# Performance work log

Measured on AMD Instinct MI355X. Metric: run time of the kernel, lower is better.

The kernel has to match this reference:

```python
import jax, jax.numpy as jnp
import numpy as np

B, N, ND_, FEAT, WV = 32, 1024, 8, 2048, 300
E, T, STEPS = 20000, 2, 5
NDIM = N * ND_  # 8192


def setup_inputs() -> dict:
    key = jax.random.key(0)
    ks = jax.random.split(key, 20)
    s = 0.02
    inputs = jax.random.normal(ks[0], (B, FEAT), jnp.float32)
    wordvecs = jax.random.normal(ks[1], (N, WV), jnp.float32)
    # unique edges per type (disjoint across types) so the scatter has no duplicate indices
    rng = np.random.default_rng(0)
    codes = rng.permutation(N * N)[: T * E].reshape(T, E)
    edge_u = (codes // N).astype(np.int32)
    edge_v = (codes % N).astype(np.int32)
    ki = np.repeat(np.arange(ND_), ND_)
    kj = np.tile(np.arange(ND_), ND_)
    mat_u = (edge_u.reshape(-1)[:, None] * ND_ + ki[None, :]).reshape(-1).astype(np.int32)
    mat_v = (edge_v.reshape(-1)[:, None] * ND_ + kj[None, :]).reshape(-1).astype(np.int32)
    p = {
        'inputs': inputs, 'wordvecs': wordvecs,
        'edge_u': jnp.asarray(edge_u), 'edge_v': jnp.asarray(edge_v),
        'mat_u': jnp.asarray(mat_u), 'mat_v': jnp.asarray(mat_v),
        # Inputnet: Linear(feat+wv -> 512), Linear(512 -> node_dim)
        'W_in1': jax.random.normal(ks[2], (512, FEAT + WV), jnp.float32) * s,
        'b_in1': jnp.zeros((512,), jnp.float32),
        'W_in2': jax.random.normal(ks[3], (ND_, 512), jnp.float32) * s,
        'b_in2': jnp.zeros((ND_,), jnp.float32),
        # embnet: Linear(wv -> 50)
        'W_emb': jax.random.normal(ks[4], (50, WV), jnp.float32) * s,
        'b_emb': jnp.zeros((50,), jnp.float32),
        # relnets: one (50, 50*nd^2) matrix per edge type
        'rel_mats': jax.random.normal(ks[5], (T, 50, 50 * ND_ * ND_), jnp.float32) * s,
        # GRUCell(node_dim, node_dim)
        'W_ih': jax.random.normal(ks[6], (3 * ND_, ND_), jnp.float32) * s,
        'W_hh': jax.random.normal(ks[7], (3 * ND_, ND_), jnp.float32) * s,
        'b_ih': jnp.zeros((3 * ND_,), jnp.float32),
        'b_hh': jnp.zeros((3 * ND_,), jnp.float32),
        # outnet: Linear(nd -> 20), ReLU, Linear(20 -> 1)
        'W_o1': jax.random.normal(ks[8], (20, ND_), jnp.float32) * s,
        'b_o1': jnp.zeros((20,), jnp.float32),
        'W_o2': jax.random.normal(ks[9], (1, 20), jnp.float32) * s,
        'b_o2': jnp.zeros((1,), jnp.float32),
    }
    return p


def reference(inputs, wordvecs, edge_u, edge_v, mat_u, mat_v,
              W_in1, b_in1, W_in2, b_in2, W_emb, b_emb, rel_mats,
              W_ih, W_hh, b_ih, b_hh, W_o1, b_o1, W_o2, b_o2):
    nd = W_in2.shape[0]
    n_nodes = wordvecs.shape[0]
    ndim = n_nodes * nd
    bsz = inputs.shape[0]

    # Inputnet: per-(image, node) feature -> initial hidden state [B, N*nd]
    f = jnp.concatenate([
        jnp.broadcast_to(inputs[:, None, :], (bsz, n_nodes, inputs.shape[1])),
        jnp.broadcast_to(wordvecs[None, :, :], (bsz, n_nodes, wordvecs.shape[1])),
    ], axis=-1).reshape(bsz * n_nodes, -1)
    h = jax.nn.relu(f @ W_in1.T + b_in1) @ W_in2.T + b_in2  # [B*N, nd]
    hidden = h.reshape(bsz, ndim)

    # edge weights via Relnet per edge type
    embs = wordvecs @ W_emb.T + b_emb  # [N, 50]
    ws = []
    for t in range(rel_mats.shape[0]):
        ue = embs[edge_u[t]]  # [E, 50]
        ve = embs[edge_v[t]]  # [E, 50]
        tmp = (ue @ rel_mats[t]).reshape(ue.shape[0], embs.shape[1], nd * nd)
        ws.append(jnp.einsum('ed,edk->ek', ve, tmp))  # [E, nd^2]
    weights = jnp.concatenate(ws, axis=0).reshape(-1)

    # scatter into dense propagation matrix
    P = jnp.zeros((ndim, ndim), jnp.float32).at[mat_u, mat_v].set(weights)
    norm = jnp.sqrt(jnp.sum(P * P, axis=1))  # row L2 norms [ndim]
    norm = norm + (norm == 0).astype(P.dtype)
    P = P / norm  # NOTE: torch broadcasting divides COLUMNS by row norms (faithful)

    def gru(x, hc):
        gi = x @ W_ih.T + b_ih
        gh = hc @ W_hh.T + b_hh
        ir, iz, inn = jnp.split(gi, 3, axis=-1)
        hr, hz, hn = jnp.split(gh, 3, axis=-1)
        r = jax.nn.sigmoid(ir + hr)
        z = jax.nn.sigmoid(iz + hz)
        n = jnp.tanh(inn + r * hn)
        return (1.0 - z) * n + z * hc

    hiddens = [hidden]
    for _ in range(STEPS):
        x = jnp.tanh(hidden @ P.T)  # [B, ndim]
        hidden = gru(x.reshape(-1, nd), hidden.reshape(-1, nd)).reshape(bsz, ndim)
        hiddens.append(hidden)
    states = jnp.stack(hiddens, axis=1)  # [B, STEPS+1, ndim]

    o = jax.nn.relu(states.reshape(-1, nd) @ W_o1.T + b_o1) @ W_o2.T + b_o2  # [B*(S+1)*N, 1]
    logits = o.reshape(bsz, STEPS + 1, n_nodes).transpose(0, 2, 1)  # [B, N, S+1]
    return logits
```

## Files before the change

kernel.cpp:

```cpp
#include <hip/hip_runtime.h>
#include <math.h>

constexpr int B = 32, N = 1024, ND = 8, FEAT = 2048, WVD = 300;
constexpr int E = 20000, T = 2, STEPS = 5;
constexpr int NDIM = N * ND;
constexpr int H1 = 512;
constexpr int W1C = FEAT + WVD;
constexpr int EMB = 50;
constexpr int RC = EMB * ND * ND;
constexpr int KH = 150;
constexpr int CAP = 64;
constexpr int SEG = 16;
constexpr int SEGLEN = E / SEG;

constexpr int G_KA   = 512;
constexpr int G_W1T  = 16 * 10;
constexpr int G_EMB  = N * 25 / 4;
constexpr int G_SEGH = T * N * SEG / 4;
constexpr int F1_TOT = G_KA + G_W1T + G_EMB + G_SEGH;

constexpr int G_ARED = 8;
constexpr int G_WV   = 512;
constexpr int G_AHAT = 13 * 32 * T;
constexpr int F2_TOT = G_ARED + G_WV + G_AHAT;

constexpr int G_SCAT = T * N * SEG / 4;
constexpr int F3_TOT = G_SCAT + N;

__global__ __launch_bounds__(256) void k_f1(
        const int* eu, int* segcnt,
        const float* inp, const float* W1, float* partA, float* W1T,
        const float* wv, const float* We, const float* be,
        float* embs, float* embsT) {
    __shared__ float smem[8 * 260];
    int tid = threadIdx.x;
    int blk = blockIdx.x;
    if (blk < G_KA) {
        int c = tid & 7, b = tid >> 3;
        int c0 = (blk & 63) * 8;
        int ks = blk >> 6;
        int kt = ks * 256;
        {
            int r = tid >> 5, cb = (tid & 31) * 8;
            const float* src = W1 + (size_t)(c0 + r) * W1C + kt + cb;
            float4 a0 = *(const float4*)src;
            float4 a1 = *(const float4*)(src + 4);
            *(float4*)&smem[r * 260 + cb] = a0;
            *(float4*)&smem[r * 260 + cb + 4] = a1;
        }
        __syncthreads();
        const float* xr = inp + (size_t)b * FEAT + kt;
        float acc = 0.f;
#pragma unroll 8
        for (int k4 = 0; k4 < 64; k4++) {
            float4 x = *(const float4*)(xr + k4 * 4);
            float4 w = *(const float4*)&smem[c * 260 + k4 * 4];
            acc += x.x * w.x + x.y * w.y + x.z * w.z + x.w * w.w;
        }
        partA[(size_t)ks * (H1 * B) + (c0 + c) * B + b] = acc;
    } else if (blk < G_KA + G_W1T) {
        int lb = blk - G_KA;
        int c0 = (lb % 16) * 32, k0 = (lb / 16) * 32;
        float (*tile)[33] = (float(*)[33])smem;
        int kl = tid & 31, cl4 = tid >> 5;
#pragma unroll
        for (int p = 0; p < 4; p++) {
            int c = cl4 + p * 8;
            int k = k0 + kl;
            if (k < WVD) tile[c][kl] = W1[(size_t)(c0 + c) * W1C + FEAT + k];
        }
        __syncthreads();
        int cl = tid & 31, kl4 = tid >> 5;
#pragma unroll
        for (int p = 0; p < 4; p++) {
            int kk = kl4 + p * 8;
            int k = k0 + kk;
            if (k < WVD) W1T[(size_t)k * H1 + c0 + cl] = tile[cl][kk];
        }
    } else if (blk < G_KA + G_W1T + G_EMB) {
        int lb = blk - G_KA - G_W1T;
        int wid = lb * 4 + (tid >> 6);
        int lane = tid & 63;
        int n = wid / 25, cp = wid - n * 25;
        int c0 = cp * 2;
        const float* xr = wv + (size_t)n * WVD;
        const float* wr0 = We + (size_t)c0 * WVD;
        const float* wr1 = wr0 + WVD;
        float a0 = 0.f, a1 = 0.f;
#pragma unroll
        for (int i = 0; i < 5; i++) {
            int k = i * 64 + lane;
            if (k < WVD) {
                float x = xr[k];
                a0 += x * wr0[k];
                a1 += x * wr1[k];
            }
        }
        for (int m = 32; m; m >>= 1) {
            a0 += __shfl_xor(a0, m, 64);
            a1 += __shfl_xor(a1, m, 64);
        }
        if (lane == 0) {
            float v0 = a0 + be[c0], v1 = a1 + be[c0 + 1];
            embs[n * EMB + c0] = v0;
            embs[n * EMB + c0 + 1] = v1;
            embsT[c0 * N + n] = v0;
            embsT[(c0 + 1) * N + n] = v1;
        }
    } else {
        int lb = blk - G_KA - G_W1T - G_EMB;
        int wid = lb * 4 + (tid >> 6);
        int lane = tid & 63;
        int t = wid >> 14, u = (wid >> 4) & (N - 1), seg = wid & (SEG - 1);
        const int* eut = eu + t * E;
        int e0 = seg * SEGLEN, e1 = e0 + SEGLEN, cnt = 0;
        for (int c = e0; c < e1; c += 64) {
            int e = c + lane;
            bool ok = (e < e1) && (eut[e] == u);
            cnt += __popcll(__ballot(ok));
        }
        if (lane == 0) segcnt[wid] = cnt;
    }
}

__global__ __launch_bounds__(256) void k_f2(
        const float* partA, float* AbT,
        const float* wv, const float* W1T, float* Wp,
        const float* embsT, const float* RMbase, float* Ahat) {
    __shared__ float smemf[1800];
    int tid = threadIdx.x, blk = blockIdx.x;
    if (blk < G_ARED) {
        int cb = blk * 2048 + tid * 8;
        float4 s0 = {0, 0, 0, 0}, s1 = {0, 0, 0, 0};
#pragma unroll
        for (int ks = 0; ks < 8; ks++) {
            const float* p = partA + (size_t)ks * (H1 * B) + cb;
            float4 a = *(const float4*)p;
            float4 b4 = *(const float4*)(p + 4);
            s0.x += a.x; s0.y += a.y; s0.z += a.z; s0.w += a.w;
            s1.x += b4.x; s1.y += b4.y; s1.z += b4.z; s1.w += b4.w;
        }
        *(float4*)(AbT + cb) = s0;
        *(float4*)(AbT + cb + 4) = s1;
    } else if (blk < G_ARED + G_WV) {
        int lb = blk - G_ARED;
        int kh = lb >> 8;
        int rem = lb & 255;
        int c = (rem & 1) * 256 + tid;
        int n0 = (rem >> 1) * 8;
        int kb = kh * KH;
        float (*el)[8] = (float(*)[8])smemf;
        for (int idx = tid; idx < 8 * KH; idx += 256) {
            int j = idx / KH, k = idx - j * KH;
            el[k][j] = wv[(size_t)(n0 + j) * WVD + kb + k];
        }
        __syncthreads();
        float acc[8] = {};
#pragma unroll 5
        for (int k = 0; k < KH; k++) {
            float r = W1T[(size_t)(kb + k) * H1 + c];
            float4 e0 = *(const float4*)&el[k][0];
            float4 e1 = *(const float4*)&el[k][4];
            acc[0] += e0.x * r; acc[1] += e0.y * r;
            acc[2] += e0.z * r; acc[3] += e0.w * r;
            acc[4] += e1.x * r; acc[5] += e1.y * r;
            acc[6] += e1.z * r; acc[7] += e1.w * r;
        }
        float* wout = Wp + (size_t)kh * N * H1;
#pragma unroll
        for (int j = 0; j < 8; j++) wout[(size_t)(n0 + j) * H1 + c] = acc[j];
    } else {
        int lb = blk - G_ARED - G_WV;
        int t = lb / 416, r = lb % 416;
        int bx = r % 13, by = r / 13;
        const float* RM = RMbase + (size_t)t * EMB * RC;
        float* Ah = Ahat + (size_t)t * N * RC;
        int n0 = by * 32;
        float (*el)[36] = (float(*)[36])smemf;
        for (int idx = tid; idx < EMB * 32; idx += 256)
            el[idx >> 5][idx & 31] = embsT[(idx >> 5) * N + n0 + (idx & 31)];
        __syncthreads();
        int mi = bx * 256 + (tid & 63) * 4;
        int ni = (tid >> 6) * 8;
        if (mi < RC) {
            float acc[8][4] = {};
#pragma unroll 2
            for (int c = 0; c < EMB; c++) {
                float4 rm = *(const float4*)(RM + (size_t)c * RC + mi);
                float4 e0 = *(const float4*)&el[c][ni];
                float4 e1 = *(const float4*)&el[c][ni + 4];
                float ev[8] = {e0.x, e0.y, e0.z, e0.w, e1.x, e1.y, e1.z, e1.w};
#pragma unroll
                for (int j = 0; j < 8; j++) {
                    acc[j][0] += ev[j] * rm.x;
                    acc[j][1] += ev[j] * rm.y;
                    acc[j][2] += ev[j] * rm.z;
                    acc[j][3] += ev[j] * rm.w;
                }
            }
#pragma unroll
            for (int j = 0; j < 8; j++) {
                float4 o = {acc[j][0], acc[j][1], acc[j][2], acc[j][3]};
                *(float4*)(Ah + (size_t)(n0 + ni + j) * RC + mi) = o;
            }
        }
    }
}

__global__ __launch_bounds__(256) void k_f3(
        const int* eu, const int* ev, const int* segcnt, int* sv,
        const float* AbT, const float* Wp, const float* b1,
        const float* W2, const float* b2, float* sT0) {
    __shared__ float smem[6656];
    int tid = threadIdx.x, blk = blockIdx.x;
    if (blk < G_SCAT) {
        int wid = blk * 4 + (tid >> 6);
        int lane = tid & 63;
        int t = wid >> 14, u = (wid >> 4) & (N - 1), seg = wid & (SEG - 1);
        const int* eut = eu + t * E;
        const int* evt = ev + t * E;
        int row = t * N + u;
        int pre = 0;
        for (int j = 0; j < seg; j++) pre += segcnt[row * SEG + j];
        int base = row * CAP + pre;
        int e0 = seg * SEGLEN, e1 = e0 + SEGLEN, cnt = 0;
        for (int c = e0; c < e1; c += 64) {
            int e = c + lane;
            bool ok = (e < e1) && (eut[e] == u);
            unsigned long long m = __ballot(ok);
            if (ok) {
                int rank = __popcll(m & ((1ull << lane) - 1));
                sv[base + cnt + rank] = evt[e];
            }
            cnt += __popcll(m);
        }
    } else {
        int n = blk - G_SCAT;
        float* w2s  = smem;
        float* wvs  = smem + 4096;
        float* part = smem + 4608;
        for (int idx = tid; idx < 8 * H1; idx += 256) w2s[idx] = W2[idx];
        for (int idx = tid; idx < H1; idx += 256)
            wvs[idx] = Wp[(size_t)n * H1 + idx]
                     + Wp[(size_t)N * H1 + (size_t)n * H1 + idx] + b1[idx];
        __syncthreads();
        int b = tid & 31, s = tid >> 5;
        float acc[8] = {};
        for (int i = 0; i < 64; i++) {
            int c = s * 64 + i;
            float tv = fmaxf(AbT[c * 32 + b] + wvs[c], 0.f);
#pragma unroll
            for (int ki = 0; ki < 8; ki++) acc[ki] += tv * w2s[ki * H1 + c];
        }
#pragma unroll
        for (int ki = 0; ki < 8; ki++) part[s * 256 + ki * 32 + b] = acc[ki];
        __syncthreads();
        int ki2 = tid >> 5, b2i = tid & 31;
        float tot = b2[ki2];
#pragma unroll
        for (int s2 = 0; s2 < 8; s2++) tot += part[s2 * 256 + ki2 * 32 + b2i];
        sT0[(size_t)n * 256 + tid] = tot;
    }
}

__global__ __launch_bounds__(256) void k_f4(
        const int* segcnt, const int* sv, int* counts,
        const float* embs, const float* Ahat, float* wbuf, float* inorm) {
    __shared__ float AL[RC];
    __shared__ int vl[T][CAP];
    __shared__ int cl[T];
    int tid = threadIdx.x;
    int u = blockIdx.x;
    int w = tid >> 6, k = tid & 63;
    if (tid < T) {
        int row = tid * N + u;
        int c = 0;
#pragma unroll
        for (int j = 0; j < SEG; j++) c += segcnt[row * SEG + j];
        cl[tid] = c;
        counts[row] = c;
    }
    __syncthreads();
    int cnts[T];
#pragma unroll
    for (int t = 0; t < T; t++) {
        cnts[t] = cl[t];
        if (tid < CAP && tid < cnts[t])
            vl[t][tid] = sv[(size_t)(t * N + u) * CAP + tid];
    }
    float ssq = 0.f;
    for (int t = 0; t < T; t++) {
        __syncthreads();
        for (int idx = tid; idx < RC; idx += 256)
            AL[idx] = Ahat[((size_t)t * N + u) * RC + idx];
        __syncthreads();
        int cnt = cnts[t];
        size_t base = (size_t)(t * N + u) * CAP;
        for (int i = w; i < cnt; i += 4) {
            int v = vl[t][i];
            const float* vr = embs + v * EMB;
            float acc = 0.f;
#pragma unroll 10
            for (int d = 0; d < EMB; d++) acc += vr[d] * AL[d * 64 + k];
            wbuf[(base + i) * 64 + k] = acc;
            ssq += acc * acc;
        }
    }
    __syncthreads();
    AL[w * 64 + k] = ssq;
    __syncthreads();
    if (tid < 64) {
        float tot = AL[tid] + AL[64 + tid] + AL[128 + tid] + AL[192 + tid];
        tot += __shfl_xor(tot, 1, 64);
        tot += __shfl_xor(tot, 2, 64);
        tot += __shfl_xor(tot, 4, 64);
        int ki = tid >> 3, kj = tid & 7;
        if (kj == 0) {
            float nv = sqrtf(tot);
            if (nv == 0.f) nv = 1.f;
            inorm[u * ND + ki] = 1.0f / nv;
        }
    }
}

__global__ __launch_bounds__(256) void k_step(
        const int* counts, const int* sv,
        const float* wbuf, const float* inorm, const float* sT, int s,
        const float* W_ih, const float* W_hh, const float* b_ih, const float* b_hh,
        const float* Wo1, const float* bo1, const float* Wo2, const float* bo2,
        float* sOut, float* out, int last) {
    __shared__ float xs[256], hs[256], hfin[256];
    __shared__ float wih[192], whh[192];
    __shared__ float w1s[160], b1s[20], w2s[20];
    __shared__ float res[8][33];
    int tid = threadIdx.x;
    int u = blockIdx.x;
    int ki = tid >> 5, b = tid & 31;
    if (tid < 192) { wih[tid] = W_ih[tid]; whh[tid] = W_hh[tid]; }
    if (last) {
        if (tid < 160) w1s[tid] = Wo1[tid];
        if (tid < 20) { b1s[tid] = bo1[tid]; w2s[tid] = Wo2[tid]; }
    }
    const float* sIn = sT + (size_t)s * NDIM * B;
    float hown = sIn[((size_t)u * 8 + ki) * B + b];
    float acc = 0.f;
    for (int t = 0; t < T; t++) {
        int row = t * N + u;
        int cnt = counts[row];
        size_t base = (size_t)row * CAP;
        int i = 0;
        for (; i + 1 < cnt; i += 2) {
            size_t s0 = base + i, s1 = base + i + 1;
            int v0 = sv[s0], v1 = sv[s1];
            const float* wp0 = wbuf + s0 * 64 + ki * 8;
            const float* wp1 = wbuf + s1 * 64 + ki * 8;
            float4 wa0 = *(const float4*)wp0;
            float4 wb0 = *(const float4*)(wp0 + 4);
            float4 wa1 = *(const float4*)wp1;
            float4 wb1 = *(const float4*)(wp1 + 4);
            const float* ip0 = inorm + v0 * ND;
            const float* ip1 = inorm + v1 * ND;
            const float* hp0 = sIn + (size_t)v0 * 256 + b;
            const float* hp1 = sIn + (size_t)v1 * 256 + b;
            acc += (wa0.x * ip0[0]) * hp0[0]   + (wa0.y * ip0[1]) * hp0[32]
                 + (wa0.z * ip0[2]) * hp0[64]  + (wa0.w * ip0[3]) * hp0[96]
                 + (wb0.x * ip0[4]) * hp0[128] + (wb0.y * ip0[5]) * hp0[160]
                 + (wb0.z * ip0[6]) * hp0[192] + (wb0.w * ip0[7]) * hp0[224];
            acc += (wa1.x * ip1[0]) * hp1[0]   + (wa1.y * ip1[1]) * hp1[32]
                 + (wa1.z * ip1[2]) * hp1[64]  + (wa1.w * ip1[3]) * hp1[96]
                 + (wb1.x * ip1[4]) * hp1[128] + (wb1.y * ip1[5]) * hp1[160]
                 + (wb1.z * ip1[6]) * hp1[192] + (wb1.w * ip1[7]) * hp1[224];
        }
        if (i < cnt) {
            size_t s0 = base + i;
            int v0 = sv[s0];
            const float* wp0 = wbuf + s0 * 64 + ki * 8;
            float4 wa0 = *(const float4*)wp0;
            float4 wb0 = *(const float4*)(wp0 + 4);
            const float* ip0 = inorm + v0 * ND;
            const float* hp0 = sIn + (size_t)v0 * 256 + b;
            acc += (wa0.x * ip0[0]) * hp0[0]   + (wa0.y * ip0[1]) * hp0[32]
                 + (wa0.z * ip0[2]) * hp0[64]  + (wa0.w * ip0[3]) * hp0[96]
                 + (wb0.x * ip0[4]) * hp0[128] + (wb0.y * ip0[5]) * hp0[160]
                 + (wb0.z * ip0[6]) * hp0[192] + (wb0.w * ip0[7]) * hp0[224];
        }
    }
    float xv = tanhf(acc);
    xs[ki * 32 + b] = xv;
    hs[ki * 32 + b] = hown;
    __syncthreads();
    float gr = b_ih[ki], gz = b_ih[8 + ki], gn = b_ih[16 + ki];
    float hr = b_hh[ki], hz = b_hh[8 + ki], hn = b_hh[16 + ki];
#pragma unroll
    for (int j = 0; j < 8; j++) {
        float xj = xs[j * 32 + b], hj = hs[j * 32 + b];
        gr += wih[ki * 8 + j] * xj;
        gz += wih[(8 + ki) * 8 + j] * xj;
        gn += wih[(16 + ki) * 8 + j] * xj;
        hr += whh[ki * 8 + j] * hj;
        hz += whh[(8 + ki) * 8 + j] * hj;
        hn += whh[(16 + ki) * 8 + j] * hj;
    }
    float r = 1.f / (1.f + expf(-(gr + hr)));
    float z = 1.f / (1.f + expf(-(gz + hz)));
    float nn = tanhf(gn + r * hn);
    float hnew = (1.f - z) * nn + z * hown;
    if (!last) {
        sOut[((size_t)u * 8 + ki) * B + b] = hnew;
        return;
    }
    hfin[ki * 32 + b] = hnew;
    __syncthreads();
    int s6 = tid >> 5, bb = tid & 31;
    if (s6 < 6) {
        float x[8];
#pragma unroll
        for (int kk = 0; kk < 8; kk++)
            x[kk] = (s6 < STEPS)
                ? sT[((size_t)s6 * NDIM + u * 8 + kk) * B + bb]
                : hfin[kk * 32 + bb];
        float accv = bo2[0];
#pragma unroll
        for (int j = 0; j < 20; j++) {
            float h = b1s[j];
#pragma unroll
            for (int kk = 0; kk < 8; kk++) h += w1s[j * 8 + kk] * x[kk];
            h = fmaxf(h, 0.f);
            accv += w2s[j] * h;
        }
        res[s6][bb] = accv;
    }
    __syncthreads();
    if (tid < 192) {
        int b_w = tid / 6, s_w = tid - b_w * 6;
        out[(size_t)b_w * ((STEPS + 1) * N) + u * (STEPS + 1) + s_w] = res[s_w][b_w];
    }
}

extern "C" void kernel_launch(void* const* d_in, const int* in_sizes, int n_in,
                              void* d_out, int out_size, void* d_ws, size_t ws_size,
                              hipStream_t stream) {
    const float* inputs   = (const float*)d_in[0];
    const float* wordvecs = (const float*)d_in[1];
    const int*   edge_u   = (const int*)d_in[2];
    const int*   edge_v   = (const int*)d_in[3];
    const float* W_in1 = (const float*)d_in[6];
    const float* b_in1 = (const float*)d_in[7];
    const float* W_in2 = (const float*)d_in[8];
    const float* b_in2 = (const float*)d_in[9];
    const float* W_emb = (const float*)d_in[10];
    const float* b_emb = (const float*)d_in[11];
    const float* rel_mats = (const float*)d_in[12];
    const float* W_ih = (const float*)d_in[13];
    const float* W_hh = (const float*)d_in[14];
    const float* b_ih = (const float*)d_in[15];
    const float* b_hh = (const float*)d_in[16];
    const float* W_o1 = (const float*)d_in[17];
    const float* b_o1 = (const float*)d_in[18];
    const float* W_o2 = (const float*)d_in[19];
    const float* b_o2 = (const float*)d_in[20];
    float* out = (float*)d_out;

    char* ws = (char*)d_ws;
    size_t off = 0;
    auto alloc = [&](size_t bytes) -> void* {
        void* p = ws + off;
        off = (off + bytes + 255) & ~(size_t)255;
        return p;
    };
    int* segcnt    = (int*)alloc((size_t)T * N * SEG * 4);
    int* counts    = (int*)alloc(2048 * 4);
    int* sv        = (int*)alloc((size_t)T * N * CAP * 4);
    float* inorm   = (float*)alloc((size_t)NDIM * 4);
    float* partA   = (float*)alloc((size_t)8 * H1 * B * 4);
    float* AbT     = (float*)alloc((size_t)H1 * B * 4);
    float* W1T     = (float*)alloc((size_t)WVD * H1 * 4);
    float* Wp      = (float*)alloc((size_t)2 * N * H1 * 4);
    float* embs    = (float*)alloc((size_t)N * EMB * 4);
    float* embsT   = (float*)alloc((size_t)EMB * N * 4);
    float* Ahat    = (float*)alloc((size_t)T * N * RC * 4);
    float* wbuf    = (float*)alloc((size_t)T * N * CAP * 64 * 4);
    float* sT      = (float*)alloc((size_t)(STEPS + 1) * NDIM * B * 4);

    k_f1<<<F1_TOT, 256, 0, stream>>>(edge_u, segcnt, inputs, W_in1, partA, W1T,
                                     wordvecs, W_emb, b_emb, embs, embsT);
    k_f2<<<F2_TOT, 256, 0, stream>>>(partA, AbT, wordvecs, W1T, Wp,
                                     embsT, rel_mats, Ahat);
    k_f3<<<F3_TOT, 256, 0, stream>>>(edge_u, edge_v, segcnt, sv,
                                     AbT, Wp, b_in1, W_in2, b_in2, sT);
    k_f4<<<N, 256, 0, stream>>>(segcnt, sv, counts, embs, Ahat, wbuf, inorm);

    for (int s = 0; s < STEPS; s++) {
        int last = (s == STEPS - 1) ? 1 : 0;
        k_step<<<N, 256, 0, stream>>>(counts, sv, wbuf, inorm, sT, s,
                                      W_ih, W_hh, b_ih, b_hh,
                                      W_o1, b_o1, W_o2, b_o2,
                                      sT + (size_t)(s + 1) * NDIM * B, out, last);
    }
}
```

Before: 265.5 us.

## Fuse edge-weight and GRU step kernels into one cooperative persistent kernel

Replaces the k_f4 launch and the five per-step k_step launches with a single cooperative kernel of 512 blocks, each handling two nodes, separated by grid-wide syncs. This removes the launch gaps between the six kernels and keeps the final hidden state in shared memory for the output MLP. k_f3's input-net tail also processes four nodes per block instead of one. In exchange, each block does twice the sequential work, grid.sync has its own cost, and the old path is kept as a fallback if the cooperative launch fails.

```diff
diff --git a/kernel.cpp b/kernel.cpp
--- a/kernel.cpp
+++ b/kernel.cpp
@@ -1,5 +1,8 @@
 #include <hip/hip_runtime.h>
+#include <hip/hip_cooperative_groups.h>
 #include <math.h>
+
+namespace cg = cooperative_groups;
 
 constexpr int B = 32, N = 1024, ND = 8, FEAT = 2048, WVD = 300;
 constexpr int E = 20000, T = 2, STEPS = 5;
@@ -12,6 +15,7 @@
 constexpr int CAP = 64;
 constexpr int SEG = 16;
 constexpr int SEGLEN = E / SEG;
+constexpr int NBLK = 512;
 
 constexpr int G_KA   = 512;
 constexpr int G_W1T  = 16 * 10;
@@ -25,7 +29,8 @@
 constexpr int F2_TOT = G_ARED + G_WV + G_AHAT;
 
 constexpr int G_SCAT = T * N * SEG / 4;
-constexpr int F3_TOT = G_SCAT + N;
+constexpr int G_INP  = N / 4;
+constexpr int F3_TOT = G_SCAT + G_INP;
 
 __global__ __launch_bounds__(256) void k_f1(
         const int* eu, int* segcnt,
@@ -235,31 +240,227 @@
             cnt += __popcll(m);
         }
     } else {
-        int n = blk - G_SCAT;
+        int n0 = (blk - G_SCAT) * 4;
         float* w2s  = smem;
         float* wvs  = smem + 4096;
         float* part = smem + 4608;
         for (int idx = tid; idx < 8 * H1; idx += 256) w2s[idx] = W2[idx];
-        for (int idx = tid; idx < H1; idx += 256)
-            wvs[idx] = Wp[(size_t)n * H1 + idx]
-                     + Wp[(size_t)N * H1 + (size_t)n * H1 + idx] + b1[idx];
-        __syncthreads();
         int b = tid & 31, s = tid >> 5;
-        float acc[8] = {};
-        for (int i = 0; i < 64; i++) {
-            int c = s * 64 + i;
-            float tv = fmaxf(AbT[c * 32 + b] + wvs[c], 0.f);
-#pragma unroll
-            for (int ki = 0; ki < 8; ki++) acc[ki] += tv * w2s[ki * H1 + c];
-        }
-#pragma unroll
-        for (int ki = 0; ki < 8; ki++) part[s * 256 + ki * 32 + b] = acc[ki];
-        __syncthreads();
         int ki2 = tid >> 5, b2i = tid & 31;
-        float tot = b2[ki2];
-#pragma unroll
-        for (int s2 = 0; s2 < 8; s2++) tot += part[s2 * 256 + ki2 * 32 + b2i];
-        sT0[(size_t)n * 256 + tid] = tot;
+        for (int nn = 0; nn < 4; nn++) {
+            int n = n0 + nn;
+            __syncthreads();
+            for (int idx = tid; idx < H1; idx += 256)
+                wvs[idx] = Wp[(size_t)n * H1 + idx]
+                         + Wp[(size_t)N * H1 + (size_t)n * H1 + idx] + b1[idx];
+            __syncthreads();
+            float acc[8] = {};
+            for (int i = 0; i < 64; i++) {
+                int c = s * 64 + i;
+                float tv = fmaxf(AbT[c * 32 + b] + wvs[c], 0.f);
+#pragma unroll
+                for (int ki = 0; ki < 8; ki++) acc[ki] += tv * w2s[ki * H1 + c];
+            }
+#pragma unroll
+            for (int ki = 0; ki < 8; ki++) part[s * 256 + ki * 32 + b] = acc[ki];
+            __syncthreads();
+            float tot = b2[ki2];
+#pragma unroll
+            for (int s2 = 0; s2 < 8; s2++) tot += part[s2 * 256 + ki2 * 32 + b2i];
+            sT0[(size_t)n * 256 + tid] = tot;
+        }
+    }
+}
+
+__device__ __forceinline__ float spmm_row(
+        const float* sIn, const int* sv, const float* wbuf, const float* inorm,
+        int row, int cnt, int ki, int b) {
+    float acc = 0.f;
+    size_t base = (size_t)row * CAP;
+    int i = 0;
+    for (; i + 1 < cnt; i += 2) {
+        size_t s0 = base + i, s1 = base + i + 1;
+        int v0 = sv[s0], v1 = sv[s1];
+        const float* wp0 = wbuf + s0 * 64 + ki * 8;
+        const float* wp1 = wbuf + s1 * 64 + ki * 8;
+        float4 wa0 = *(const float4*)wp0;
+        float4 wb0 = *(const float4*)(wp0 + 4);
+        float4 wa1 = *(const float4*)wp1;
+        float4 wb1 = *(const float4*)(wp1 + 4);
+        const float* ip0 = inorm + v0 * ND;
+        const float* ip1 = inorm + v1 * ND;
+        const float* hp0 = sIn + (size_t)v0 * 256 + b;
+        const float* hp1 = sIn + (size_t)v1 * 256 + b;
+        acc += (wa0.x * ip0[0]) * hp0[0]   + (wa0.y * ip0[1]) * hp0[32]
+             + (wa0.z * ip0[2]) * hp0[64]  + (wa0.w * ip0[3]) * hp0[96]
+             + (wb0.x * ip0[4]) * hp0[128] + (wb0.y * ip0[5]) * hp0[160]
+             + (wb0.z * ip0[6]) * hp0[192] + (wb0.w * ip0[7]) * hp0[224];
+        acc += (wa1.x * ip1[0]) * hp1[0]   + (wa1.y * ip1[1]) * hp1[32]
+             + (wa1.z * ip1[2]) * hp1[64]  + (wa1.w * ip1[3]) * hp1[96]
+             + (wb1.x * ip1[4]) * hp1[128] + (wb1.y * ip1[5]) * hp1[160]
+             + (wb1.z * ip1[6]) * hp1[192] + (wb1.w * ip1[7]) * hp1[224];
+    }
+    if (i < cnt) {
+        size_t s0 = base + i;
+        int v0 = sv[s0];
+        const float* wp0 = wbuf + s0 * 64 + ki * 8;
+        float4 wa0 = *(const float4*)wp0;
+        float4 wb0 = *(const float4*)(wp0 + 4);
+        const float* ip0 = inorm + v0 * ND;
+        const float* hp0 = sIn + (size_t)v0 * 256 + b;
+        acc += (wa0.x * ip0[0]) * hp0[0]   + (wa0.y * ip0[1]) * hp0[32]
+             + (wa0.z * ip0[2]) * hp0[64]  + (wa0.w * ip0[3]) * hp0[96]
+             + (wb0.x * ip0[4]) * hp0[128] + (wb0.y * ip0[5]) * hp0[160]
+             + (wb0.z * ip0[6]) * hp0[192] + (wb0.w * ip0[7]) * hp0[224];
+    }
+    return acc;
+}
+
+__global__ __launch_bounds__(256, 4) void k_steps(
+        const int* segcnt, const int* sv, const float* embs, const float* Ahat,
+        float* wbuf, float* inorm, float* sT,
+        const float* W_ih, const float* W_hh, const float* b_ih, const float* b_hh,
+        const float* Wo1, const float* bo1, const float* Wo2, const float* bo2,
+        float* out) {
+    cg::grid_group grid = cg::this_grid();
+    __shared__ float S[3400];
+    __shared__ int vl[T][CAP];
+    __shared__ int cl[T];
+    int tid = threadIdx.x;
+    int w = tid >> 6, k = tid & 63;
+    int cnts[2][T];
+
+    for (int half = 0; half < 2; half++) {
+        int u = blockIdx.x + half * NBLK;
+        __syncthreads();
+        if (tid < T) {
+            int row = tid * N + u;
+            int c = 0;
+#pragma unroll
+            for (int j = 0; j < SEG; j++) c += segcnt[row * SEG + j];
+            cl[tid] = c;
+        }
+        __syncthreads();
+#pragma unroll
+        for (int t = 0; t < T; t++) {
+            cnts[half][t] = cl[t];
+            if (tid < cnts[half][t]) vl[t][tid] = sv[(size_t)(t * N + u) * CAP + tid];
+        }
+        float ssq = 0.f;
+        for (int t = 0; t < T; t++) {
+            __syncthreads();
+            for (int idx = tid; idx < RC; idx += 256)
+                S[idx] = Ahat[((size_t)t * N + u) * RC + idx];
+            __syncthreads();
+            int cnt = cnts[half][t];
+            size_t base = (size_t)(t * N + u) * CAP;
+            for (int i = w; i < cnt; i += 4) {
+                int v = vl[t][i];
+                const float* vr = embs + v * EMB;
+                float acc = 0.f;
+#pragma unroll 10
+                for (int d = 0; d < EMB; d++) acc += vr[d] * S[d * 64 + k];
+                wbuf[(base + i) * 64 + k] = acc;
+                ssq += acc * acc;
+            }
+        }
+        __syncthreads();
+        S[w * 64 + k] = ssq;
+        __syncthreads();
+        if (tid < 64) {
+            float tot = S[tid] + S[64 + tid] + S[128 + tid] + S[192 + tid];
+            tot += __shfl_xor(tot, 1, 64);
+            tot += __shfl_xor(tot, 2, 64);
+            tot += __shfl_xor(tot, 4, 64);
+            int ki = tid >> 3, kj = tid & 7;
+            if (kj == 0) {
+                float nv = sqrtf(tot);
+                if (nv == 0.f) nv = 1.f;
+                inorm[u * ND + ki] = 1.0f / nv;
+            }
+        }
+    }
+    grid.sync();
+
+    float* xs   = S;
+    float* hs   = S + 256;
+    float* hfin = S + 512;
+    float* wih  = S + 1024;
+    float* whh  = S + 1216;
+    float* w1s  = S + 1408;
+    float* b1s  = S + 1568;
+    float* w2s  = S + 1588;
+    float (*res)[33] = (float(*)[33])(S + 1608);
+    if (tid < 192) { wih[tid] = W_ih[tid]; whh[tid] = W_hh[tid]; }
+    if (tid < 160) w1s[tid] = Wo1[tid];
+    if (tid < 20) { b1s[tid] = bo1[tid]; w2s[tid] = Wo2[tid]; }
+    __syncthreads();
+    int ki = tid >> 5, b = tid & 31;
+
+    for (int s = 0; s < STEPS; s++) {
+        const float* sIn = sT + (size_t)s * NDIM * B;
+        for (int half = 0; half < 2; half++) {
+            int u = blockIdx.x + half * NBLK;
+            float hown = sIn[((size_t)u * 8 + ki) * B + b];
+            float acc = spmm_row(sIn, sv, wbuf, inorm, u, cnts[half][0], ki, b)
+                      + spmm_row(sIn, sv, wbuf, inorm, N + u, cnts[half][1], ki, b);
+            float xv = tanhf(acc);
+            __syncthreads();
+            xs[ki * 32 + b] = xv;
+            hs[ki * 32 + b] = hown;
+            __syncthreads();
+            float gr = b_ih[ki], gz = b_ih[8 + ki], gn = b_ih[16 + ki];
+            float hr = b_hh[ki], hz = b_hh[8 + ki], hn = b_hh[16 + ki];
+#pragma unroll
+            for (int j = 0; j < 8; j++) {
+                float xj = xs[j * 32 + b], hj = hs[j * 32 + b];
+                gr += wih[ki * 8 + j] * xj;
+                gz += wih[(8 + ki) * 8 + j] * xj;
+                gn += wih[(16 + ki) * 8 + j] * xj;
+                hr += whh[ki * 8 + j] * hj;
+                hz += whh[(8 + ki) * 8 + j] * hj;
+                hn += whh[(16 + ki) * 8 + j] * hj;
+            }
+            float r = 1.f / (1.f + expf(-(gr + hr)));
+            float z = 1.f / (1.f + expf(-(gz + hz)));
+            float nn = tanhf(gn + r * hn);
+            float hnew = (1.f - z) * nn + z * hown;
+            if (s < STEPS - 1)
+                sT[(size_t)(s + 1) * NDIM * B + ((size_t)u * 8 + ki) * B + b] = hnew;
+            else
+                hfin[half * 256 + ki * 32 + b] = hnew;
+        }
+        if (s < STEPS - 1) grid.sync();
+    }
+    __syncthreads();
+
+    int s6 = tid >> 5, bb = tid & 31;
+    for (int half = 0; half < 2; half++) {
+        int u = blockIdx.x + half * NBLK;
+        __syncthreads();
+        if (s6 < 6) {
+            float x[8];
+#pragma unroll
+            for (int kk = 0; kk < 8; kk++)
+                x[kk] = (s6 < STEPS)
+                    ? sT[((size_t)s6 * NDIM + u * 8 + kk) * B + bb]
+                    : hfin[half * 256 + kk * 32 + bb];
+            float accv = bo2[0];
+#pragma unroll
+            for (int j = 0; j < 20; j++) {
+                float h = b1s[j];
+#pragma unroll
+                for (int kk = 0; kk < 8; kk++) h += w1s[j * 8 + kk] * x[kk];
+                h = fmaxf(h, 0.f);
+                accv += w2s[j] * h;
+            }
+            res[s6][bb] = accv;
+        }
+        __syncthreads();
+        if (tid < 192) {
+            int b_w = tid / 6, s_w = tid - b_w * 6;
+            out[(size_t)b_w * ((STEPS + 1) * N) + u * (STEPS + 1) + s_w] = res[s_w][b_w];
+        }
     }
 }
 
@@ -285,8 +486,7 @@
 #pragma unroll
     for (int t = 0; t < T; t++) {
         cnts[t] = cl[t];
-        if (tid < CAP && tid < cnts[t])
-            vl[t][tid] = sv[(size_t)(t * N + u) * CAP + tid];
+        if (tid < cnts[t]) vl[t][tid] = sv[(size_t)(t * N + u) * CAP + tid];
     }
     float ssq = 0.f;
     for (int t = 0; t < T; t++) {
@@ -343,48 +543,8 @@
     }
     const float* sIn = sT + (size_t)s * NDIM * B;
     float hown = sIn[((size_t)u * 8 + ki) * B + b];
-    float acc = 0.f;
-    for (int t = 0; t < T; t++) {
-        int row = t * N + u;
-        int cnt = counts[row];
-        size_t base = (size_t)row * CAP;
-        int i = 0;
-        for (; i + 1 < cnt; i += 2) {
-            size_t s0 = base + i, s1 = base + i + 1;
-            int v0 = sv[s0], v1 = sv[s1];
-            const float* wp0 = wbuf + s0 * 64 + ki * 8;
-            const float* wp1 = wbuf + s1 * 64 + ki * 8;
-            float4 wa0 = *(const float4*)wp0;
-            float4 wb0 = *(const float4*)(wp0 + 4);
-            float4 wa1 = *(const float4*)wp1;
-            float4 wb1 = *(const float4*)(wp1 + 4);
-            const float* ip0 = inorm + v0 * ND;
-            const float* ip1 = inorm + v1 * ND;
-            const float* hp0 = sIn + (size_t)v0 * 256 + b;
-            const float* hp1 = sIn + (size_t)v1 * 256 + b;
-            acc += (wa0.x * ip0[0]) * hp0[0]   + (wa0.y * ip0[1]) * hp0[32]
-                 + (wa0.z * ip0[2]) * hp0[64]  + (wa0.w * ip0[3]) * hp0[96]
-                 + (wb0.x * ip0[4]) * hp0[128] + (wb0.y * ip0[5]) * hp0[160]
-                 + (wb0.z * ip0[6]) * hp0[192] + (wb0.w * ip0[7]) * hp0[224];
-            acc += (wa1.x * ip1[0]) * hp1[0]   + (wa1.y * ip1[1]) * hp1[32]
-                 + (wa1.z * ip1[2]) * hp1[64]  + (wa1.w * ip1[3]) * hp1[96]
-                 + (wb1.x * ip1[4]) * hp1[128] + (wb1.y * ip1[5]) * hp1[160]
-                 + (wb1.z * ip1[6]) * hp1[192] + (wb1.w * ip1[7]) * hp1[224];
-        }
-        if (i < cnt) {
-            size_t s0 = base + i;
-            int v0 = sv[s0];
-            const float* wp0 = wbuf + s0 * 64 + ki * 8;
-            float4 wa0 = *(const float4*)wp0;
-            float4 wb0 = *(const float4*)(wp0 + 4);
-            const float* ip0 = inorm + v0 * ND;
-            const float* hp0 = sIn + (size_t)v0 * 256 + b;
-            acc += (wa0.x * ip0[0]) * hp0[0]   + (wa0.y * ip0[1]) * hp0[32]
-                 + (wa0.z * ip0[2]) * hp0[64]  + (wa0.w * ip0[3]) * hp0[96]
-                 + (wb0.x * ip0[4]) * hp0[128] + (wb0.y * ip0[5]) * hp0[160]
-                 + (wb0.z * ip0[6]) * hp0[192] + (wb0.w * ip0[7]) * hp0[224];
-        }
-    }
+    float acc = spmm_row(sIn, sv, wbuf, inorm, u, counts[u], ki, b)
+              + spmm_row(sIn, sv, wbuf, inorm, N + u, counts[N + u], ki, b);
     float xv = tanhf(acc);
     xs[ki * 32 + b] = xv;
     hs[ki * 32 + b] = hown;
@@ -488,13 +648,24 @@
                                      embsT, rel_mats, Ahat);
     k_f3<<<F3_TOT, 256, 0, stream>>>(edge_u, edge_v, segcnt, sv,
                                      AbT, Wp, b_in1, W_in2, b_in2, sT);
-    k_f4<<<N, 256, 0, stream>>>(segcnt, sv, counts, embs, Ahat, wbuf, inorm);
-
-    for (int s = 0; s < STEPS; s++) {
-        int last = (s == STEPS - 1) ? 1 : 0;
-        k_step<<<N, 256, 0, stream>>>(counts, sv, wbuf, inorm, sT, s,
-                                      W_ih, W_hh, b_ih, b_hh,
-                                      W_o1, b_o1, W_o2, b_o2,
-                                      sT + (size_t)(s + 1) * NDIM * B, out, last);
-    }
-}
+
+    void* args[] = {
+        (void*)&segcnt, (void*)&sv, (void*)&embs, (void*)&Ahat,
+        (void*)&wbuf, (void*)&inorm, (void*)&sT,
+        (void*)&W_ih, (void*)&W_hh, (void*)&b_ih, (void*)&b_hh,
+        (void*)&W_o1, (void*)&b_o1, (void*)&W_o2, (void*)&b_o2,
+        (void*)&out
+    };
+    hipError_t cerr = hipLaunchCooperativeKernel((const void*)k_steps, dim3(NBLK),
+                                                 dim3(256), args, 0, stream);
+    if (cerr != hipSuccess) {
+        k_f4<<<N, 256, 0, stream>>>(segcnt, sv, counts, embs, Ahat, wbuf, inorm);
+        for (int s = 0; s < STEPS; s++) {
+            int last = (s == STEPS - 1) ? 1 : 0;
+            k_step<<<N, 256, 0, stream>>>(counts, sv, wbuf, inorm, sT, s,
+                                          W_ih, W_hh, b_ih, b_hh,
+                                          W_o1, b_o1, W_o2, b_o2,
+                                          sT + (size_t)(s + 1) * NDIM * B, out, last);
+        }
+    }
+}
```

Result: slower. 653.5 us (+146.2%).

## Fuse edge scatter into per-node weight kernel and skip empty segments

Applied to the files above, without the earlier changes.

Merges the edge-list compaction pass into the per-node relation-weight kernel, so each node block builds its neighbour list in shared memory, scans only the segments that hold edges, and then computes wbuf and inorm without a separate launch. The count pass now uses 50 segments instead of 16, which makes each segment shorter and lets empty ones be skipped. The input-net blocks now process four nodes each. The aim is to remove one kernel launch, the global round trip of sv, and redundant scans over empty segments. In exchange the count pass launches more work and the fused blocks do the scan and the matvec serially.

```diff
diff --git a/kernel.cpp b/kernel.cpp
--- a/kernel.cpp
+++ b/kernel.cpp
@@ -10,7 +10,7 @@
 constexpr int RC = EMB * ND * ND;
 constexpr int KH = 150;
 constexpr int CAP = 64;
-constexpr int SEG = 16;
+constexpr int SEG = 50;
 constexpr int SEGLEN = E / SEG;
 
 constexpr int G_KA   = 512;
@@ -24,8 +24,8 @@
 constexpr int G_AHAT = 13 * 32 * T;
 constexpr int F2_TOT = G_ARED + G_WV + G_AHAT;
 
-constexpr int G_SCAT = T * N * SEG / 4;
-constexpr int F3_TOT = G_SCAT + N;
+constexpr int G_INP  = N / 4;
+constexpr int F3_TOT = N + G_INP;
 
 __global__ __launch_bounds__(256) void k_f1(
         const int* eu, int* segcnt,
@@ -111,7 +111,9 @@
         int lb = blk - G_KA - G_W1T - G_EMB;
         int wid = lb * 4 + (tid >> 6);
         int lane = tid & 63;
-        int t = wid >> 14, u = (wid >> 4) & (N - 1), seg = wid & (SEG - 1);
+        int t = wid / (N * SEG);
+        int rem = wid - t * (N * SEG);
+        int u = rem / SEG, seg = rem - u * SEG;
         const int* eut = eu + t * E;
         int e0 = seg * SEGLEN, e1 = e0 + SEGLEN, cnt = 0;
         for (int c = e0; c < e1; c += 64) {
@@ -119,7 +121,7 @@
             bool ok = (e < e1) && (eut[e] == u);
             cnt += __popcll(__ballot(ok));
         }
-        if (lane == 0) segcnt[wid] = cnt;
+        if (lane == 0) segcnt[(t * N + u) * SEG + seg] = cnt;
     }
 }
 
@@ -208,117 +210,132 @@
 }
 
 __global__ __launch_bounds__(256) void k_f3(
-        const int* eu, const int* ev, const int* segcnt, int* sv,
+        const int* eu, const int* ev, const int* segcnt,
+        const float* embs, const float* Ahat, float* wbuf, float* inorm,
+        int* counts, int* sv,
         const float* AbT, const float* Wp, const float* b1,
         const float* W2, const float* b2, float* sT0) {
     __shared__ float smem[6656];
-    int tid = threadIdx.x, blk = blockIdx.x;
-    if (blk < G_SCAT) {
-        int wid = blk * 4 + (tid >> 6);
-        int lane = tid & 63;
-        int t = wid >> 14, u = (wid >> 4) & (N - 1), seg = wid & (SEG - 1);
-        const int* eut = eu + t * E;
-        const int* evt = ev + t * E;
-        int row = t * N + u;
-        int pre = 0;
-        for (int j = 0; j < seg; j++) pre += segcnt[row * SEG + j];
-        int base = row * CAP + pre;
-        int e0 = seg * SEGLEN, e1 = e0 + SEGLEN, cnt = 0;
-        for (int c = e0; c < e1; c += 64) {
-            int e = c + lane;
-            bool ok = (e < e1) && (eut[e] == u);
-            unsigned long long m = __ballot(ok);
-            if (ok) {
-                int rank = __popcll(m & ((1ull << lane) - 1));
-                sv[base + cnt + rank] = evt[e];
-            }
-            cnt += __popcll(m);
+    int tid = threadIdx.x;
+    int blk = blockIdx.x;
+    if (blk < N) {
+        int u = blk;
+        float* AL   = smem;
+        int* vl     = (int*)(smem + 3328);
+        int* scnt   = vl + T * CAP;
+        int* soff   = scnt + T * SEG;
+        int* slist  = soff + T * SEG;
+        int* smeta  = slist + T * SEG;
+        int w = tid >> 6, lane = tid & 63;
+        if (tid < T * SEG) {
+            int t = tid / SEG, s = tid - t * SEG;
+            scnt[tid] = segcnt[((size_t)t * N + u) * SEG + s];
+        }
+        __syncthreads();
+        if (w < T && lane == 0) {
+            int off = 0, nn = 0;
+            for (int j = 0; j < SEG; j++) {
+                int c = scnt[w * SEG + j];
+                soff[w * SEG + j] = off;
+                off += c;
+                if (c > 0) slist[w * SEG + nn++] = j;
+            }
+            smeta[w] = nn;
+            smeta[T + w] = off;
+            counts[w * N + u] = off;
+        }
+        __syncthreads();
+        {
+            int myrow = w >> 1, sub = w & 1;
+            int row = myrow * N + u;
+            const int* eut = eu + myrow * E;
+            const int* evt = ev + myrow * E;
+            int nnz = smeta[myrow];
+            for (int idx = sub; idx < nnz; idx += 2) {
+                int seg = slist[myrow * SEG + idx];
+                int base = soff[myrow * SEG + seg];
+                int e0 = seg * SEGLEN, e1 = e0 + SEGLEN, cnt = 0;
+                for (int c = e0; c < e1; c += 64) {
+                    int e = c + lane;
+                    bool ok = (e < e1) && (eut[e] == u);
+                    unsigned long long m = __ballot(ok);
+                    if (ok) {
+                        int rank = __popcll(m & ((1ull << lane) - 1));
+                        int pos = base + cnt + rank;
+                        vl[myrow * CAP + pos] = evt[e];
+                        sv[(size_t)row * CAP + pos] = evt[e];
+                    }
+                    cnt += __popcll(m);
+                }
+            }
+        }
+        __syncthreads();
+        int cnts[T];
+#pragma unroll
+        for (int t = 0; t < T; t++) cnts[t] = smeta[T + t];
+        int k = lane;
+        float ssq = 0.f;
+        for (int t = 0; t < T; t++) {
+            __syncthreads();
+            for (int idx = tid; idx < RC; idx += 256)
+                AL[idx] = Ahat[((size_t)t * N + u) * RC + idx];
+            __syncthreads();
+            int cnt = cnts[t];
+            size_t base = (size_t)(t * N + u) * CAP;
+            for (int i = w; i < cnt; i += 4) {
+                int v = vl[t * CAP + i];
+                const float* vr = embs + v * EMB;
+                float acc = 0.f;
+#pragma unroll 10
+                for (int d = 0; d < EMB; d++) acc += vr[d] * AL[d * 64 + k];
+                wbuf[(base + i) * 64 + k] = acc;
+                ssq += acc * acc;
+            }
+        }
+        __syncthreads();
+        AL[w * 64 + k] = ssq;
+        __syncthreads();
+        if (tid < 64) {
+            float tot = AL[tid] + AL[64 + tid] + AL[128 + tid] + AL[192 + tid];
+            tot += __shfl_xor(tot, 1, 64);
+            tot += __shfl_xor(tot, 2, 64);
+            tot += __shfl_xor(tot, 4, 64);
+            int ki = tid >> 3, kj = tid & 7;
+            if (kj == 0) {
+                float nv = sqrtf(tot);
+                if (nv == 0.f) nv = 1.f;
+                inorm[u * ND + ki] = 1.0f / nv;
+            }
         }
     } else {
-        int n = blk - G_SCAT;
+        int n0 = (blk - N) * 4;
         float* w2s  = smem;
         float* wvs  = smem + 4096;
         float* part = smem + 4608;
         for (int idx = tid; idx < 8 * H1; idx += 256) w2s[idx] = W2[idx];
-        for (int idx = tid; idx < H1; idx += 256)
-            wvs[idx] = Wp[(size_t)n * H1 + idx]
-                     + Wp[(size_t)N * H1 + (size_t)n * H1 + idx] + b1[idx];
-        __syncthreads();
         int b = tid & 31, s = tid >> 5;
-        float acc[8] = {};
-        for (int i = 0; i < 64; i++) {
-            int c = s * 64 + i;
-            float tv = fmaxf(AbT[c * 32 + b] + wvs[c], 0.f);
-#pragma unroll
-            for (int ki = 0; ki < 8; ki++) acc[ki] += tv * w2s[ki * H1 + c];
-        }
-#pragma unroll
-        for (int ki = 0; ki < 8; ki++) part[s * 256 + ki * 32 + b] = acc[ki];
-        __syncthreads();
         int ki2 = tid >> 5, b2i = tid & 31;
-        float tot = b2[ki2];
-#pragma unroll
-        for (int s2 = 0; s2 < 8; s2++) tot += part[s2 * 256 + ki2 * 32 + b2i];
-        sT0[(size_t)n * 256 + tid] = tot;
-    }
-}
-
-__global__ __launch_bounds__(256) void k_f4(
-        const int* segcnt, const int* sv, int* counts,
-        const float* embs, const float* Ahat, float* wbuf, float* inorm) {
-    __shared__ float AL[RC];
-    __shared__ int vl[T][CAP];
-    __shared__ int cl[T];
-    int tid = threadIdx.x;
-    int u = blockIdx.x;
-    int w = tid >> 6, k = tid & 63;
-    if (tid < T) {
-        int row = tid * N + u;
-        int c = 0;
-#pragma unroll
-        for (int j = 0; j < SEG; j++) c += segcnt[row * SEG + j];
-        cl[tid] = c;
-        counts[row] = c;
-    }
-    __syncthreads();
-    int cnts[T];
-#pragma unroll
-    for (int t = 0; t < T; t++) {
-        cnts[t] = cl[t];
-        if (tid < CAP && tid < cnts[t])
-            vl[t][tid] = sv[(size_t)(t * N + u) * CAP + tid];
-    }
-    float ssq = 0.f;
-    for (int t = 0; t < T; t++) {
-        __syncthreads();
-        for (int idx = tid; idx < RC; idx += 256)
-            AL[idx] = Ahat[((size_t)t * N + u) * RC + idx];
-        __syncthreads();
-        int cnt = cnts[t];
-        size_t base = (size_t)(t * N + u) * CAP;
-        for (int i = w; i < cnt; i += 4) {
-            int v = vl[t][i];
-            const float* vr = embs + v * EMB;
-            float acc = 0.f;
-#pragma unroll 10
-            for (int d = 0; d < EMB; d++) acc += vr[d] * AL[d * 64 + k];
-            wbuf[(base + i) * 64 + k] = acc;
-            ssq += acc * acc;
-        }
-    }
-    __syncthreads();
-    AL[w * 64 + k] = ssq;
-    __syncthreads();
-    if (tid < 64) {
-        float tot = AL[tid] + AL[64 + tid] + AL[128 + tid] + AL[192 + tid];
-        tot += __shfl_xor(tot, 1, 64);
-        tot += __shfl_xor(tot, 2, 64);
-        tot += __shfl_xor(tot, 4, 64);
-        int ki = tid >> 3, kj = tid & 7;
-        if (kj == 0) {
-            float nv = sqrtf(tot);
-            if (nv == 0.f) nv = 1.f;
-            inorm[u * ND + ki] = 1.0f / nv;
+        for (int nn = 0; nn < 4; nn++) {
+            int n = n0 + nn;
+            __syncthreads();
+            for (int idx = tid; idx < H1; idx += 256)
+                wvs[idx] = Wp[(size_t)n * H1 + idx]
+                         + Wp[(size_t)N * H1 + (size_t)n * H1 + idx] + b1[idx];
+            __syncthreads();
+            float acc[8] = {};
+            for (int i = 0; i < 64; i++) {
+                int c = s * 64 + i;
+                float tv = fmaxf(AbT[c * 32 + b] + wvs[c], 0.f);
+#pragma unroll
+                for (int ki = 0; ki < 8; ki++) acc[ki] += tv * w2s[ki * H1 + c];
+            }
+#pragma unroll
+            for (int ki = 0; ki < 8; ki++) part[s * 256 + ki * 32 + b] = acc[ki];
+            __syncthreads();
+            float tot = b2[ki2];
+#pragma unroll
+            for (int s2 = 0; s2 < 8; s2++) tot += part[s2 * 256 + ki2 * 32 + b2i];
+            sT0[(size_t)n * 256 + tid] = tot;
         }
     }
 }
@@ -486,9 +503,9 @@
                                      wordvecs, W_emb, b_emb, embs, embsT);
     k_f2<<<F2_TOT, 256, 0, stream>>>(partA, AbT, wordvecs, W1T, Wp,
                                      embsT, rel_mats, Ahat);
-    k_f3<<<F3_TOT, 256, 0, stream>>>(edge_u, edge_v, segcnt, sv,
+    k_f3<<<F3_TOT, 256, 0, stream>>>(edge_u, edge_v, segcnt,
+                                     embs, Ahat, wbuf, inorm, counts, sv,
                                      AbT, Wp, b_in1, W_in2, b_in2, sT);
-    k_f4<<<N, 256, 0, stream>>>(segcnt, sv, counts, embs, Ahat, wbuf, inorm);
 
     for (int s = 0; s < STEPS; s++) {
         int last = (s == STEPS - 1) ? 1 : 0;
```

New measurement: 242.6 us. -8.6%, faster.
